# Kernel optimization log

Hardware: AMD Instinct MI355X
Metric: run time of the kernel (lower is better)

The kernel has to match this reference:

```python
import jax, jax.numpy as jnp
import numpy as np


def _zoom(x, k, n):
    # x: [B, C, T, F]; zoom frequency axis by factor n/k via linear interpolation.
    # output[..., f] = w * x[..., floor(f*k/n)] + (1-w) * x[..., floor(f*k/n)+1]
    # where w = 1 - frac(f*k/n); out-of-range source indices contribute 0.
    if n == k:
        return x
    F_ = x.shape[3]
    f = jnp.arange(F_)
    pos = f * k                     # integer numerator of f*k/n
    idx = pos // n                  # floor(f*k/n)
    frac = (pos % n).astype(x.dtype) / jnp.asarray(n, x.dtype)
    w = 1.0 - frac                  # weight for lower neighbor, shape [F]
    if n == 1:
        # strided gather + zero pad (pure decimation, w == 1 everywhere)
        valid = idx < F_
        x0 = jnp.take(x, jnp.clip(idx, 0, F_ - 1), axis=3)
        return jnp.where(valid, x0, jnp.zeros((), x.dtype))
    valid0 = idx < F_
    valid1 = (idx + 1) < F_
    x0 = jnp.take(x, jnp.clip(idx, 0, F_ - 1), axis=3)
    x1 = jnp.take(x, jnp.clip(idx + 1, 0, F_ - 1), axis=3)
    out = jnp.where(valid0, w * x0, jnp.zeros((), x.dtype)) \
        + jnp.where(valid1, (1.0 - w) * x1, jnp.zeros((), x.dtype))
    return out


def setup_inputs() -> dict:
    key = jax.random.key(0)
    x = jax.random.normal(key, (8, 16, 256, 1024), dtype=jnp.float32)
    return {"input": x, "k": 2, "n": 3}


def reference(input, k, n):
    return _zoom(input, k, n)
```

## Files before the change

kernel.cpp:

```cpp
#include <hip/hip_runtime.h>


typedef float f32x4 __attribute__((ext_vector_type(4)));

constexpr int F = 1024;
constexpr int VEC = 4;
constexpr int BLOCK = F / VEC;
constexpr int RU = 4;

__global__ __launch_bounds__(BLOCK) void zoom_kernel(
    const float* __restrict__ x,
    const int* __restrict__ kp,
    const int* __restrict__ np_,
    float* __restrict__ out,
    int nrows) {
  __shared__ float lds[2][RU][F];

  const int k = kp[0];
  const int n = np_[0];

  const int f0 = threadIdx.x * VEC;
  const int wv = threadIdx.x >> 6;
  const int ln = threadIdx.x & 63;

  int  idx0[VEC], idx1[VEC];
  float w0[VEC], w1[VEC];
#pragma unroll
  for (int j = 0; j < VEC; ++j) {
    const int f   = f0 + j;
    const int pos = f * k;
    const int id  = pos / n;
    const int rem = pos - id * n;
    const float w = 1.0f - (float)rem / (float)n;
    const bool v0 = id < F;
    const bool v1 = (id + 1) < F;
    w0[j]   = v0 ? w : 0.0f;
    w1[j]   = v1 ? (1.0f - w) : 0.0f;
    idx0[j] = v0 ? id : 0;
    idx1[j] = v1 ? (id + 1) : (F - 1);
  }

  int nwords = ((F - 1) * k) / n + 2;
  if (nwords > F) nwords = F;
  const int segs = (nwords + 255) >> 8;
  const int nstage = RU * segs;

  const int nchunks = (nrows + RU - 1) / RU;

  auto stage = [&](int chunk, int buf) {
    const size_t row0 = (size_t)chunk * RU;
    for (int s = wv; s < nstage; s += 4) {
      const int r   = s / segs;
      const int seg = s - r * segs;
      size_t row = row0 + (size_t)r;
      if (row >= (size_t)nrows) row = (size_t)nrows - 1;
      const float* gp = x + row * F + seg * 256 + ln * 4;
      float* lp = &lds[buf][r][seg * 256];
      __builtin_amdgcn_global_load_lds(
          (const __attribute__((address_space(1))) void*)gp,
          (__attribute__((address_space(3))) void*)lp, 16, 0, 0);
    }
  };

  const int c0 = blockIdx.x;
  int cur = 0;
  if (c0 < nchunks) stage(c0, 0);
  __syncthreads();

  for (int c = c0; c < nchunks; c += gridDim.x) {
    const int cn = c + gridDim.x;
    if (cn < nchunks) stage(cn, cur ^ 1);

    const size_t row0 = (size_t)c * RU;
#pragma unroll
    for (int r = 0; r < RU; ++r) {
      if (row0 + (size_t)r >= (size_t)nrows) break;
      f32x4 v;
      v.x = w0[0] * lds[cur][r][idx0[0]] + w1[0] * lds[cur][r][idx1[0]];
      v.y = w0[1] * lds[cur][r][idx0[1]] + w1[1] * lds[cur][r][idx1[1]];
      v.z = w0[2] * lds[cur][r][idx0[2]] + w1[2] * lds[cur][r][idx1[2]];
      v.w = w0[3] * lds[cur][r][idx0[3]] + w1[3] * lds[cur][r][idx1[3]];
      __builtin_nontemporal_store(v, (f32x4*)(out + (row0 + (size_t)r) * F + f0));
    }

    __syncthreads();
    cur ^= 1;
  }
}

extern "C" void kernel_launch(void* const* d_in, const int* in_sizes, int n_in,
                              void* d_out, int out_size, void* d_ws, size_t ws_size,
                              hipStream_t stream) {
  const float* x   = (const float*)d_in[0];
  const int*   kp  = (const int*)d_in[1];
  const int*   np_ = (const int*)d_in[2];
  float* out = (float*)d_out;

  const int total = in_sizes[0];
  const int nrows = total / F;

  const int nchunks = (nrows + RU - 1) / RU;
  const int grid = (nchunks < 2048) ? nchunks : 2048;
  zoom_kernel<<<grid, BLOCK, 0, stream>>>(x, kp, np_, out, nrows);
}
```

Measured before the change: 40.45 us.

## Replace persistent double-buffered loop with one-chunk-per-block launch and trimmed staging

Drops the persistent grid-stride loop and its LDS double buffer. The kernel now launches one block per 4-row chunk and stages only that chunk, which halves LDS per block and removes the per-iteration barriers. The last staged segment is shifted back so it ends at the needed words instead of loading a full 256-word segment past them, trimming redundant global reads. In exchange it relies on many resident blocks for latency hiding instead of explicit prefetch, and it launches more blocks.

```diff
diff --git a/kernel.cpp b/kernel.cpp
--- a/kernel.cpp
+++ b/kernel.cpp
@@ -14,7 +14,7 @@
     const int* __restrict__ np_,
     float* __restrict__ out,
     int nrows) {
-  __shared__ float lds[2][RU][F];
+  __shared__ float lds[RU][F];
 
   const int k = kp[0];
   const int n = np_[0];
@@ -43,48 +43,37 @@
   int nwords = ((F - 1) * k) / n + 2;
   if (nwords > F) nwords = F;
   const int segs = (nwords + 255) >> 8;
+  int last_start = 0;
+  if (nwords > 256) {
+    last_start = (nwords - 256 + 3) & ~3;
+  }
   const int nstage = RU * segs;
 
-  const int nchunks = (nrows + RU - 1) / RU;
+  const size_t row0 = (size_t)blockIdx.x * RU;
 
-  auto stage = [&](int chunk, int buf) {
-    const size_t row0 = (size_t)chunk * RU;
-    for (int s = wv; s < nstage; s += 4) {
-      const int r   = s / segs;
-      const int seg = s - r * segs;
-      size_t row = row0 + (size_t)r;
-      if (row >= (size_t)nrows) row = (size_t)nrows - 1;
-      const float* gp = x + row * F + seg * 256 + ln * 4;
-      float* lp = &lds[buf][r][seg * 256];
-      __builtin_amdgcn_global_load_lds(
-          (const __attribute__((address_space(1))) void*)gp,
-          (__attribute__((address_space(3))) void*)lp, 16, 0, 0);
-    }
-  };
-
-  const int c0 = blockIdx.x;
-  int cur = 0;
-  if (c0 < nchunks) stage(c0, 0);
+  for (int s = wv; s < nstage; s += 4) {
+    const int r   = s / segs;
+    const int seg = s - r * segs;
+    const int start = (seg == segs - 1) ? last_start : seg * 256;
+    size_t row = row0 + (size_t)r;
+    if (row >= (size_t)nrows) row = (size_t)nrows - 1;
+    const float* gp = x + row * F + start + ln * 4;
+    float* lp = &lds[r][start];
+    __builtin_amdgcn_global_load_lds(
+        (const __attribute__((address_space(1))) void*)gp,
+        (__attribute__((address_space(3))) void*)lp, 16, 0, 0);
+  }
   __syncthreads();
 
-  for (int c = c0; c < nchunks; c += gridDim.x) {
-    const int cn = c + gridDim.x;
-    if (cn < nchunks) stage(cn, cur ^ 1);
-
-    const size_t row0 = (size_t)c * RU;
 #pragma unroll
-    for (int r = 0; r < RU; ++r) {
-      if (row0 + (size_t)r >= (size_t)nrows) break;
-      f32x4 v;
-      v.x = w0[0] * lds[cur][r][idx0[0]] + w1[0] * lds[cur][r][idx1[0]];
-      v.y = w0[1] * lds[cur][r][idx0[1]] + w1[1] * lds[cur][r][idx1[1]];
-      v.z = w0[2] * lds[cur][r][idx0[2]] + w1[2] * lds[cur][r][idx1[2]];
-      v.w = w0[3] * lds[cur][r][idx0[3]] + w1[3] * lds[cur][r][idx1[3]];
-      __builtin_nontemporal_store(v, (f32x4*)(out + (row0 + (size_t)r) * F + f0));
-    }
-
-    __syncthreads();
-    cur ^= 1;
+  for (int r = 0; r < RU; ++r) {
+    if (row0 + (size_t)r >= (size_t)nrows) break;
+    f32x4 v;
+    v.x = w0[0] * lds[r][idx0[0]] + w1[0] * lds[r][idx1[0]];
+    v.y = w0[1] * lds[r][idx0[1]] + w1[1] * lds[r][idx1[1]];
+    v.z = w0[2] * lds[r][idx0[2]] + w1[2] * lds[r][idx1[2]];
+    v.w = w0[3] * lds[r][idx0[3]] + w1[3] * lds[r][idx1[3]];
+    __builtin_nontemporal_store(v, (f32x4*)(out + (row0 + (size_t)r) * F + f0));
   }
 }
 
@@ -99,7 +88,6 @@
   const int total = in_sizes[0];
   const int nrows = total / F;
 
-  const int nchunks = (nrows + RU - 1) / RU;
-  const int grid = (nchunks < 2048) ? nchunks : 2048;
+  const int grid = (nrows + RU - 1) / RU;
   zoom_kernel<<<grid, BLOCK, 0, stream>>>(x, kp, np_, out, nrows);
 }
```

Result: faster. 39.42 us (-2.5%).
